# Kernel optimization log

Hardware: AMD Instinct MI355X
Metric: run time of the kernel (lower is better)

Reference implementation:

```python
import jax, jax.numpy as jnp
import numpy as np

B, T, N, D, H = 8, 24, 512, 128, 8
HD = D // H
HID = int(D * 2.0)
SCALES = (1.0, 0.01)


def _l2norm(a):
    # F.normalize(dim=-1), eps=1e-12
    n = jnp.sqrt(jnp.sum(a * a, axis=-1, keepdims=True))
    return a / jnp.maximum(n, 1e-12)


def _layernorm(a, g, b):
    mu = a.mean(-1, keepdims=True)
    var = ((a - mu) ** 2).mean(-1, keepdims=True)
    return (a - mu) / jnp.sqrt(var + 1e-5) * g + b


def _fast_attention_layer(z, qkv_w, out_w, out_b):
    # z: [B,T,N,D]; qkv_w: [D,3D]; out_w: [2D,D]; out_b: [D]
    b, t, n, d = z.shape
    q, k, v = jnp.split(z @ qkv_w, 3, axis=-1)          # each [B,T,N,D]
    q = q.reshape(b, t, n, H, HD)
    k = k.reshape(b, t, n, H, HD)
    v = v.reshape(b, t, n, H, HD)
    qn = _l2norm(q)
    kn = _l2norm(k)
    # spatial linear attention (tokens = nodes, axis 2)
    kvs = jnp.einsum('btnhm,btnhd->bthmd', kn, v)
    num = jnp.einsum('btnhm,bthmd->btnhd', qn, kvs) + n * v
    den = jnp.einsum('btnhm,bthm->btnh', qn, kn.sum(axis=2))[..., None] + n
    out_s = (num / den).reshape(b, t, n, d)
    # temporal linear attention (tokens = time steps, axis 1)
    kvt = jnp.einsum('btnhm,btnhd->bnhmd', kn, v)
    numt = jnp.einsum('btnhm,bnhmd->btnhd', qn, kvt) + t * v
    dent = jnp.einsum('btnhm,bnhm->btnh', qn, kn.sum(axis=1))[..., None] + t
    out_t = (numt / dent).reshape(b, t, n, d)
    return jnp.concatenate([out_s, out_t], axis=-1) @ out_w + out_b


def setup_inputs() -> dict:
    key = jax.random.key(0)
    ks = jax.random.split(key, 20)
    s = 0.02
    inp = {
        'x': jax.random.normal(ks[0], (B, T, N, D), jnp.float32),
        'graph': jax.random.uniform(ks[1], (T, N, N), jnp.float32) / N,
        'qkv_w0': jax.random.normal(ks[2], (D, 3 * D), jnp.float32) * s,
        'out_w0': jax.random.normal(ks[3], (2 * D, D), jnp.float32) * s,
        'out_b0': jnp.zeros((D,), jnp.float32),
        'pw_w0': jax.random.normal(ks[4], (D, D), jnp.float32) * s,
        'pw_b0': jax.random.normal(ks[5], (D,), jnp.float32) * s,
        'qkv_w1': jax.random.normal(ks[6], (D, 3 * D), jnp.float32) * s,
        'out_w1': jax.random.normal(ks[7], (2 * D, D), jnp.float32) * s,
        'out_b1': jnp.zeros((D,), jnp.float32),
        'pw_w1': jax.random.normal(ks[8], (D, D), jnp.float32) * s,
        'pw_b1': jax.random.normal(ks[9], (D,), jnp.float32) * s,
        'fc1_w': jax.random.normal(ks[10], (D, HID), jnp.float32) * s,
        'fc1_b': jnp.zeros((HID,), jnp.float32),
        'fc2_w': jax.random.normal(ks[11], (HID, D), jnp.float32) * s,
        'fc2_b': jnp.zeros((D,), jnp.float32),
        'ln1_g': jnp.ones((D,), jnp.float32),
        'ln1_b': jnp.zeros((D,), jnp.float32),
        'ln2_g': jnp.ones((D,), jnp.float32),
        'ln2_b': jnp.zeros((D,), jnp.float32),
    }
    return inp


def reference(x, graph, qkv_w0, out_w0, out_b0, pw_w0, pw_b0,
              qkv_w1, out_w1, out_b1, pw_w1, pw_b1,
              fc1_w, fc1_b, fc2_w, fc2_b, ln1_g, ln1_b, ln2_g, ln2_b):
    # GraphPropagate (Ks=order=2): x_loc = [x, graph @ x]; dropout in eval mode
    x1 = jnp.einsum('tni,btid->btnd', graph, x)
    x_loc = (x, x1)
    layer_params = ((qkv_w0, out_w0, out_b0, pw_w0, pw_b0),
                    (qkv_w1, out_w1, out_b1, pw_w1, pw_b1))
    c = x
    x_glo = x
    for k in range(2):
        qkv_w, out_w, out_b, pw_w, pw_b = layer_params[k]
        att = _fast_attention_layer(x_loc[k], qkv_w, out_w, out_b)
        pw = c @ pw_w + pw_b
        x_glo = x_glo + att * pw * SCALES[k]
        c = att
    h = _layernorm(x + x_glo, ln1_g, ln1_b)
    mlp = jax.nn.relu(h @ fc1_w + fc1_b) @ fc2_w + fc2_b
    return _layernorm(h + mlp, ln2_g, ln2_b)
```

## Files before the change

### kernel.cpp

```cpp
#include <hip/hip_runtime.h>
#include <cstddef>

#define Bb 8
#define Tt 24
#define Nn 512
#define Dd 128
#define Hh 8

typedef unsigned short u16;
using short8 = __attribute__((ext_vector_type(8))) short;
using f32x4  = __attribute__((ext_vector_type(4))) float;

__device__ __forceinline__ float b2f(u16 u) {
  union { unsigned u; float f; } w; w.u = ((unsigned)u) << 16; return w.f;
}
__device__ __forceinline__ u16 f2b(float f) {
  union { float f; unsigned u; } w; w.f = f;
  unsigned r = w.u + 0x7FFFu + ((w.u >> 16) & 1u);
  return (u16)(r >> 16);
}

__device__ __forceinline__ void gld16(const u16* g, u16* s) {
  __builtin_amdgcn_global_load_lds(
      (const __attribute__((address_space(1))) unsigned int*)g,
      (__attribute__((address_space(3))) unsigned int*)s, 16, 0, 0);
}

__device__ __forceinline__ void mm_phase(const u16* __restrict__ A,
                                         const u16* __restrict__ BT,
                                         int K, int m0,
                                         u16* sA, u16* sB, f32x4 acc[4][4])
{
  const int tid = threadIdx.x;
  const int l = tid & 63, wid = tid >> 6;
  const int wm = (wid >> 1) << 6, wn = (wid & 1) << 6;
  int a_off[4], b_off[4];
#pragma unroll
  for (int i = 0; i < 4; ++i) {
    a_off[i] = (wm + i * 16 + (l & 15)) * 64 + (l >> 4) * 16;
    b_off[i] = (wn + i * 16 + (l & 15)) * 64 + (l >> 4) * 16;
  }
  const int gr = l >> 2, kqo = (l & 3) * 8;
  const int R0 = wid * 32 + gr, R1 = wid * 32 + 16 + gr;
  u16* dA0 = sA + (wid * 2 + 0) * 512;
  u16* dA1 = sA + (wid * 2 + 1) * 512;
  u16* dB0 = sB + (wid * 2 + 0) * 512;
  u16* dB1 = sB + (wid * 2 + 1) * 512;
  const size_t aR0 = (size_t)(m0 + R0) * K, aR1 = (size_t)(m0 + R1) * K;
  const size_t bR0 = (size_t)R0 * K, bR1 = (size_t)R1 * K;
  for (int k0 = 0; k0 < K; k0 += 32) {
    __syncthreads();
    gld16(A + aR0 + k0 + kqo, dA0);
    gld16(A + aR1 + k0 + kqo, dA1);
    gld16(BT + bR0 + k0 + kqo, dB0);
    gld16(BT + bR1 + k0 + kqo, dB1);
    __syncthreads();
    short8 af[4], bf_[4];
#pragma unroll
    for (int i = 0; i < 4; ++i) {
      af[i]  = *(const short8*)((const char*)sA + a_off[i]);
      bf_[i] = *(const short8*)((const char*)sB + b_off[i]);
    }
#pragma unroll
    for (int mi = 0; mi < 4; ++mi)
#pragma unroll
      for (int ni = 0; ni < 4; ++ni)
        acc[mi][ni] = __builtin_amdgcn_mfma_f32_16x16x32_bf16(
            af[mi], bf_[ni], acc[mi][ni], 0, 0, 0);
  }
}

template <int OUTBF16, int RELU>
__device__ __forceinline__ void gemm_mfma_body(
    const u16* __restrict__ A, const u16* __restrict__ BT,
    const float* __restrict__ bias, void* __restrict__ Cv,
    int N, int K, int m0, int n0)
{
  __shared__ u16 sA[4096];
  __shared__ u16 sB[4096];
  f32x4 acc[4][4] = {};
  mm_phase(A, BT + (size_t)n0 * K, K, m0, sA, sB, acc);
  const int l = threadIdx.x & 63, wid = threadIdx.x >> 6;
  const int wm = (wid >> 1) << 6, wn = (wid & 1) << 6;
  const int cr = (l >> 4) << 2, cc = l & 15;
#pragma unroll
  for (int mi = 0; mi < 4; ++mi) {
    int rowb = m0 + wm + mi * 16 + cr;
#pragma unroll
    for (int ni = 0; ni < 4; ++ni) {
      int col = n0 + wn + ni * 16 + cc;
      float bb = bias ? bias[col] : 0.f;
#pragma unroll
      for (int r = 0; r < 4; ++r) {
        float v = acc[mi][ni][r] + bb;
        if (RELU) v = fmaxf(v, 0.f);
        size_t idx = (size_t)(rowb + r) * N + col;
        if (OUTBF16) ((u16*)Cv)[idx] = f2b(v);
        else         ((float*)Cv)[idx] = v;
      }
    }
  }
}

template <int OUTBF16, int RELU>
__global__ __launch_bounds__(256) void gemm_mfma_k(
    const u16* __restrict__ A, const u16* __restrict__ BT,
    const float* __restrict__ bias, void* __restrict__ C, int N, int K)
{
  gemm_mfma_body<OUTBF16, RELU>(A, BT, bias, C, N, K,
                                blockIdx.y * 128, blockIdx.x * 128);
}

__global__ __launch_bounds__(256) void gemm_mfma_graph(
    const u16* __restrict__ g, const u16* __restrict__ xT, u16* __restrict__ x1)
{
  const int bt = blockIdx.z, t = bt % Tt;
  gemm_mfma_body<1, 0>(g + (size_t)t * Nn * Nn, xT + (size_t)bt * Dd * Nn,
                       nullptr, x1 + (size_t)bt * Nn * Dd,
                       Dd, Nn, blockIdx.y * 128, 0);
}

__global__ __launch_bounds__(256) void gemm_og0(
    const u16* __restrict__ cat, const u16* __restrict__ outT, const float* __restrict__ ob,
    const u16* __restrict__ xb,  const u16* __restrict__ pwT,  const float* __restrict__ pb,
    u16* __restrict__ gp0, u16* __restrict__ att0)
{
  __shared__ u16 sA[4096], sB[4096];
  const int m0 = blockIdx.x * 128;
  f32x4 accP[4][4] = {};
  mm_phase(xb, pwT, 128, m0, sA, sB, accP);
  f32x4 accO[4][4] = {};
  mm_phase(cat, outT, 256, m0, sA, sB, accO);
  const int l = threadIdx.x & 63, wid = threadIdx.x >> 6;
  const int wm = (wid >> 1) << 6, wn = (wid & 1) << 6;
  const int cr = (l >> 4) << 2, cc = l & 15;
#pragma unroll
  for (int mi = 0; mi < 4; ++mi) {
    int rowb = m0 + wm + mi * 16 + cr;
#pragma unroll
    for (int ni = 0; ni < 4; ++ni) {
      int col = wn + ni * 16 + cc;
      float obv = ob[col], pbv = pb[col];
#pragma unroll
      for (int r = 0; r < 4; ++r) {
        size_t idx = (size_t)(rowb + r) * 128 + col;
        float attv = accO[mi][ni][r] + obv;
        float pwv  = accP[mi][ni][r] + pbv;
        att0[idx] = f2b(attv);
        gp0[idx] = f2b(attv * pwv);
      }
    }
  }
}

__global__ __launch_bounds__(256) void gemm_og1(
    const u16* __restrict__ cat, const u16* __restrict__ outT, const float* __restrict__ ob,
    const u16* __restrict__ att0, const u16* __restrict__ pwT, const float* __restrict__ pb,
    const u16* __restrict__ gp0, const float* __restrict__ x,
    const float* __restrict__ g, const float* __restrict__ be,
    u16* __restrict__ h16)
{
  __shared__ __align__(16) u16 smem[128 * 136];
  __shared__ float sg[128], sbt[128];
  u16* sA = smem;
  u16* sB = smem + 4096;
  if (threadIdx.x < 128) { sg[threadIdx.x] = g[threadIdx.x]; sbt[threadIdx.x] = be[threadIdx.x]; }
  const int m0 = blockIdx.x * 128;
  f32x4 accP[4][4] = {};
  mm_phase(att0, pwT, 128, m0, sA, sB, accP);
  f32x4 accO[4][4] = {};
  mm_phase(cat, outT, 256, m0, sA, sB, accO);
  const int l = threadIdx.x & 63, wid = threadIdx.x >> 6;
  const int wm = (wid >> 1) << 6, wn = (wid & 1) << 6;
  const int cr = (l >> 4) << 2, cc = l & 15;
  __syncthreads();
#pragma unroll
  for (int mi = 0; mi < 4; ++mi) {
    int lrow = wm + mi * 16 + cr;
#pragma unroll
    for (int ni = 0; ni < 4; ++ni) {
      int col = wn + ni * 16 + cc;
      float obv = ob[col], pbv = pb[col];
#pragma unroll
      for (int r = 0; r < 4; ++r) {
        size_t idx = (size_t)(m0 + lrow + r) * 128 + col;
        float attv = accO[mi][ni][r] + obv;
        float pwv  = accP[mi][ni][r] + pbv;
        float hpre = 2.f * x[idx] + b2f(gp0[idx]) + attv * pwv * 0.01f;
        smem[(lrow + r) * 136 + col] = f2b(hpre);
      }
    }
  }
  __syncthreads();
  const int row = threadIdx.x >> 1, half = threadIdx.x & 1;
  const u16* rp = smem + row * 136 + half * 64;
  float s = 0.f, ss = 0.f;
#pragma unroll
  for (int j8 = 0; j8 < 8; ++j8) {
    short8 v = *(const short8*)(rp + j8 * 8);
#pragma unroll
    for (int j = 0; j < 8; ++j) { float f = b2f((u16)v[j]); s += f; ss += f * f; }
  }
  s += __shfl_xor(s, 1);
  ss += __shfl_xor(ss, 1);
  float mu = s * (1.f / 128.f);
  float rstd = rsqrtf(ss * (1.f / 128.f) - mu * mu + 1e-5f);
  size_t gbase = (size_t)(m0 + row) * 128 + half * 64;
#pragma unroll
  for (int j8 = 0; j8 < 8; ++j8) {
    short8 v = *(const short8*)(rp + j8 * 8);
    short8 o;
#pragma unroll
    for (int j = 0; j < 8; ++j) {
      int col = half * 64 + j8 * 8 + j;
      o[j] = (short)f2b((b2f((u16)v[j]) - mu) * rstd * sg[col] + sbt[col]);
    }
    *(short8*)(h16 + gbase + j8 * 8) = o;
  }
}

__global__ __launch_bounds__(256) void gemm_fc2ln(
    const u16* __restrict__ hid, const u16* __restrict__ fc2T, const float* __restrict__ fb,
    const u16* __restrict__ h16, const float* __restrict__ g, const float* __restrict__ be,
    float* __restrict__ out)
{
  __shared__ __align__(16) u16 smem[128 * 136];
  __shared__ float sg[128], sbt[128];
  u16* sA = smem;
  u16* sB = smem + 4096;
  if (threadIdx.x < 128) { sg[threadIdx.x] = g[threadIdx.x]; sbt[threadIdx.x] = be[threadIdx.x]; }
  const int m0 = blockIdx.x * 128;
  f32x4 accO[4][4] = {};
  mm_phase(hid, fc2T, 256, m0, sA, sB, accO);
  const int l = threadIdx.x & 63, wid = threadIdx.x >> 6;
  const int wm = (wid >> 1) << 6, wn = (wid & 1) << 6;
  const int cr = (l >> 4) << 2, cc = l & 15;
  __syncthreads();
#pragma unroll
  for (int mi = 0; mi < 4; ++mi) {
    int lrow = wm + mi * 16 + cr;
#pragma unroll
    for (int ni = 0; ni < 4; ++ni) {
      int col = wn + ni * 16 + cc;
      float fbv = fb[col];
#pragma unroll
      for (int r = 0; r < 4; ++r) {
        size_t idx = (size_t)(m0 + lrow + r) * 128 + col;
        float hpre = b2f(h16[idx]) + accO[mi][ni][r] + fbv;
        smem[(lrow + r) * 136 + col] = f2b(hpre);
      }
    }
  }
  __syncthreads();
  const int row = threadIdx.x >> 1, half = threadIdx.x & 1;
  const u16* rp = smem + row * 136 + half * 64;
  float s = 0.f, ss = 0.f;
#pragma unroll
  for (int j8 = 0; j8 < 8; ++j8) {
    short8 v = *(const short8*)(rp + j8 * 8);
#pragma unroll
    for (int j = 0; j < 8; ++j) { float f = b2f((u16)v[j]); s += f; ss += f * f; }
  }
  s += __shfl_xor(s, 1);
  ss += __shfl_xor(ss, 1);
  float mu = s * (1.f / 128.f);
  float rstd = rsqrtf(ss * (1.f / 128.f) - mu * mu + 1e-5f);
  size_t gbase = (size_t)(m0 + row) * 128 + half * 64;
#pragma unroll
  for (int j8 = 0; j8 < 8; ++j8) {
    short8 v = *(const short8*)(rp + j8 * 8);
    float4 o0, o1;
#pragma unroll
    for (int j = 0; j < 8; ++j) {
      int col = half * 64 + j8 * 8 + j;
      float y = (b2f((u16)v[j]) - mu) * rstd * sg[col] + sbt[col];
      if (j < 4) ((float*)&o0)[j] = y; else ((float*)&o1)[j - 4] = y;
    }
    *(float4*)(out + gbase + j8 * 8) = o0;
    *(float4*)(out + gbase + j8 * 8 + 4) = o1;
  }
}

__global__ __launch_bounds__(256) void qknorm(const u16* __restrict__ qkv,
                                              float* __restrict__ inv, size_t nidx)
{
  size_t idx = (size_t)blockIdx.x * 256 + threadIdx.x;
  if (idx >= nidx) return;
  size_t row = idx >> 4;
  int g = (int)(idx & 15);
  const u16* p = qkv + row * 384 + g * 16;
  short8 a = *(const short8*)p;
  short8 b = *(const short8*)(p + 8);
  float ss = 0.f;
#pragma unroll
  for (int j = 0; j < 8; ++j) {
    float f0 = b2f((u16)a[j]), f1 = b2f((u16)b[j]);
    ss += f0 * f0 + f1 * f1;
  }
  inv[idx] = 1.f / fmaxf(sqrtf(ss), 1e-12f);
}

__global__ __launch_bounds__(256) void cvt_f32_bf16(const float* __restrict__ src,
                                                    u16* __restrict__ dst, size_t n8)
{
  size_t i = (size_t)blockIdx.x * 256 + threadIdx.x;
  if (i >= n8) return;
  const float4* s = (const float4*)src;
  float4 u = s[i * 2], v = s[i * 2 + 1];
  short8 o;
  o[0] = (short)f2b(u.x); o[1] = (short)f2b(u.y);
  o[2] = (short)f2b(u.z); o[3] = (short)f2b(u.w);
  o[4] = (short)f2b(v.x); o[5] = (short)f2b(v.y);
  o[6] = (short)f2b(v.z); o[7] = (short)f2b(v.w);
  *(short8*)(dst + i * 8) = o;
}

__global__ __launch_bounds__(256) void transpose_cvt(const float* __restrict__ src,
                                                     u16* __restrict__ dst,
                                                     int R, int C)
{
  __shared__ u16 tile[64][65];
  const int tid = threadIdx.x;
  src += (size_t)blockIdx.z * R * C;
  dst += (size_t)blockIdx.z * R * C;
  const int c0 = blockIdx.x * 64, r0 = blockIdx.y * 64;
  const int tx = tid & 63, ty = tid >> 6;
#pragma unroll
  for (int i = 0; i < 64; i += 4)
    tile[ty + i][tx] = f2b(src[(size_t)(r0 + ty + i) * C + c0 + tx]);
  __syncthreads();
#pragma unroll
  for (int i = 0; i < 64; i += 4)
    dst[(size_t)(c0 + ty + i) * R + r0 + tx] = tile[tx][ty + i];
}

__global__ __launch_bounds__(256) void cvt_transpose_x(const float* __restrict__ src,
                                                       u16* __restrict__ xb,
                                                       u16* __restrict__ xT)
{
  __shared__ u16 tile[64][65];
  const int tid = threadIdx.x;
  const size_t zo = (size_t)blockIdx.z * Nn * Dd;
  src += zo; xb += zo; xT += zo;
  const int c0 = blockIdx.x * 64, r0 = blockIdx.y * 64;
  const int tx = tid & 63, ty = tid >> 6;
#pragma unroll
  for (int i = 0; i < 64; i += 4) {
    u16 b = f2b(src[(size_t)(r0 + ty + i) * Dd + c0 + tx]);
    tile[ty + i][tx] = b;
    xb[(size_t)(r0 + ty + i) * Dd + c0 + tx] = b;
  }
  __syncthreads();
#pragma unroll
  for (int i = 0; i < 64; i += 4)
    xT[(size_t)(c0 + ty + i) * Nn + r0 + tx] = tile[tx][ty + i];
}

__global__ __launch_bounds__(256) void spatial_stats(const u16* __restrict__ qkv,
                                                     const float* __restrict__ qkn,
                                                     float* __restrict__ kvs2,
                                                     float* __restrict__ ksum)
{
  __shared__ u16 sKT[16 * 512];
  __shared__ u16 sVT[16 * 512];
  __shared__ float red[4][16][16];
  __shared__ float red2[4][16];
  const int bt = blockIdx.x, h = blockIdx.y;
  const int tid = threadIdx.x;

  u16 kr[2][16], vr[2][16];
#pragma unroll
  for (int r = 0; r < 2; ++r) {
    int n = tid * 2 + r;
    size_t rowg = (size_t)bt * 512 + n;
    size_t base = rowg * 384;
    float inv = qkn[rowg * 16 + 8 + h];
    short8 k0 = *(const short8*)(qkv + base + 128 + h * 16);
    short8 k1 = *(const short8*)(qkv + base + 136 + h * 16);
    short8 v0 = *(const short8*)(qkv + base + 256 + h * 16);
    short8 v1 = *(const short8*)(qkv + base + 264 + h * 16);
#pragma unroll
    for (int j = 0; j < 8; ++j) {
      kr[r][j]     = f2b(b2f((u16)k0[j]) * inv);
      kr[r][j + 8] = f2b(b2f((u16)k1[j]) * inv);
      vr[r][j] = (u16)v0[j]; vr[r][j + 8] = (u16)v1[j];
    }
  }
#pragma unroll
  for (int m = 0; m < 16; ++m) {
    unsigned pk = (unsigned)kr[0][m] | ((unsigned)kr[1][m] << 16);
    unsigned pv = (unsigned)vr[0][m] | ((unsigned)vr[1][m] << 16);
    int wa = ((m << 10) + (tid << 2)) ^ ((m & 7) << 4);
    *(unsigned*)((char*)sKT + wa) = pk;
    *(unsigned*)((char*)sVT + wa) = pv;
  }
  __syncthreads();

  const int l = tid & 63, w = tid >> 6;
  const int fr = l & 15, tq = l >> 4;
  short8 ones;
#pragma unroll
  for (int j = 0; j < 8; ++j) ones[j] = (short)0x3F80;
  f32x4 acc = {}, acs = {};
#pragma unroll
  for (int kk = 0; kk < 4; ++kk) {
    int noff = w * 128 + kk * 32 + tq * 8;
    int ra = ((fr << 10) + (noff << 1)) ^ ((fr & 7) << 4);
    short8 afr = *(const short8*)((const char*)sKT + ra);
    short8 bfr = *(const short8*)((const char*)sVT + ra);
    acc = __builtin_amdgcn_mfma_f32_16x16x32_bf16(afr, bfr, acc, 0, 0, 0);
    acs = __builtin_amdgcn_mfma_f32_16x16x32_bf16(afr, ones, acs, 0, 0, 0);
  }
#pragma unroll
  for (int r = 0; r < 4; ++r) red[w][tq * 4 + r][fr] = acc[r];
  if (fr == 0) {
#pragma unroll
    for (int r = 0; r < 4; ++r) red2[w][tq * 4 + r] = acs[r];
  }
  __syncthreads();
  const size_t o = (size_t)bt * 8 + h;
  {
    int m = tid >> 4, d = tid & 15;
    float s = red[0][m][d] + red[1][m][d] + red[2][m][d] + red[3][m][d];
    kvs2[o * 256 + d * 16 + m] = s;
  }
  if (tid < 16) {
    float s = red2[0][tid] + red2[1][tid] + red2[2][tid] + red2[3][tid];
    ksum[o * 16 + tid] = s;
  }
}

__global__ __launch_bounds__(256) void temporal_stats(const u16* __restrict__ qkv,
                                                      const float* __restrict__ qkn,
                                                      float* __restrict__ kvt,
                                                      float* __restrict__ kst)
{
  __shared__ u16 sKT[128 * 32];
  __shared__ u16 sVT[128 * 32];
  const int nn = blockIdx.x, b = blockIdx.y;
  const int tid = threadIdx.x;
  if (tid < 128) {
    short8 z = {};
    int wa = ((tid << 6) + 48) ^ ((tid & 3) << 4);
    *(short8*)((char*)sKT + wa) = z;
    *(short8*)((char*)sVT + wa) = z;
  }
  for (int idx = tid; idx < 384; idx += 256) {
    int t = idx >> 4, c8 = idx & 15;
    size_t rowg = ((size_t)(b * 24 + t) * 512) + nn;
    float inv = qkn[rowg * 16 + 8 + (c8 >> 1)];
    short8 kv = *(const short8*)(qkv + rowg * 384 + 128 + c8 * 8);
    short8 vv = *(const short8*)(qkv + rowg * 384 + 256 + c8 * 8);
#pragma unroll
    for (int j = 0; j < 8; ++j) {
      int c = c8 * 8 + j;
      int wa = ((c << 6) + (t << 1)) ^ ((c & 3) << 4);
      *(u16*)((char*)sKT + wa) = f2b(b2f((u16)kv[j]) * inv);
      *(u16*)((char*)sVT + wa) = (u16)vv[j];
    }
  }
  __syncthreads();
  const int l = tid & 63, w = tid >> 6;
  const int fr = l & 15, tq = l >> 4;
  const size_t nb = (size_t)b * 512 + nn;
  short8 ones;
#pragma unroll
  for (int j = 0; j < 8; ++j) ones[j] = (short)0x3F80;
#pragma unroll
  for (int hi = 0; hi < 2; ++hi) {
    int h = w * 2 + hi;
    int c = h * 16 + fr;
    int ra = ((c << 6) + (tq << 4)) ^ ((c & 3) << 4);
    short8 afr = *(const short8*)((const char*)sKT + ra);
    short8 bfr = *(const short8*)((const char*)sVT + ra);
    f32x4 z = {};
    f32x4 acc = __builtin_amdgcn_mfma_f32_16x16x32_bf16(afr, bfr, z, 0, 0, 0);
    f32x4 acs = __builtin_amdgcn_mfma_f32_16x16x32_bf16(afr, ones, z, 0, 0, 0);
#pragma unroll
    for (int r = 0; r < 4; ++r)
      kvt[nb * 2048 + (size_t)(tq * 4 + r) * 128 + h * 16 + fr] = acc[r];
    if (fr == 0) {
#pragma unroll
      for (int r = 0; r < 4; ++r)
        kst[(nb * 8 + h) * 16 + tq * 4 + r] = acs[r];
    }
  }
}

__global__ __launch_bounds__(256) void attn_apply(const u16* __restrict__ qkv,
                                                  const float* __restrict__ qkn,
                                                  const float* __restrict__ kvs2,
                                                  const float* __restrict__ kss,
                                                  const float* __restrict__ kvt,
                                                  const float* __restrict__ kst,
                                                  u16* __restrict__ out_cat)
{
  __shared__ float s_kvt[2][2048];
  const int nn0 = blockIdx.x * 2, b = blockIdx.y;
  const int t0 = blockIdx.z * 8;
  const int tid = threadIdx.x;
  const int sub = tid >> 7, cl = tid & 127;
  const int nn = nn0 + sub;
  const size_t nb = (size_t)b * 512 + nn;
  for (int i = cl; i < 2048; i += 128) s_kvt[sub][i] = kvt[nb * 2048 + i];
  __syncthreads();
  const int hh = cl >> 4, d = cl & 15;
  float kstr[16];
  {
    const float4* k4 = (const float4*)(kst + (nb * 8 + hh) * 16);
#pragma unroll
    for (int i = 0; i < 4; ++i) {
      float4 v = k4[i];
      kstr[i * 4] = v.x; kstr[i * 4 + 1] = v.y; kstr[i * 4 + 2] = v.z; kstr[i * 4 + 3] = v.w;
    }
  }
  for (int t = t0; t < t0 + 8; ++t) {
    const size_t row = ((size_t)(b * 24 + t) * 512) + nn;
    const u16* qp = qkv + row * 384 + hh * 16;
    short8 q0 = *(const short8*)qp;
    short8 q1 = *(const short8*)(qp + 8);
    const float inv = qkn[row * 16 + hh];
    float qf[16];
#pragma unroll
    for (int j = 0; j < 8; ++j) {
      qf[j] = b2f((u16)q0[j]);
      qf[j + 8] = b2f((u16)q1[j]);
    }
    const size_t hb = (size_t)(b * 24 + t) * 8 + hh;
    const float4* M4 = (const float4*)(kvs2 + hb * 256 + d * 16);
    float accs = 0.f;
#pragma unroll
    for (int i = 0; i < 4; ++i) {
      float4 m = M4[i];
      accs = fmaf(qf[i * 4], m.x, fmaf(qf[i * 4 + 1], m.y,
             fmaf(qf[i * 4 + 2], m.z, fmaf(qf[i * 4 + 3], m.w, accs))));
    }
    const float4* K4 = (const float4*)(kss + hb * 16);
    float dps = 0.f;
#pragma unroll
    for (int i = 0; i < 4; ++i) {
      float4 m = K4[i];
      dps = fmaf(qf[i * 4], m.x, fmaf(qf[i * 4 + 1], m.y,
            fmaf(qf[i * 4 + 2], m.z, fmaf(qf[i * 4 + 3], m.w, dps))));
    }
    float acct = 0.f, dpt = 0.f;
#pragma unroll
    for (int mI = 0; mI < 16; ++mI) {
      acct = fmaf(qf[mI], s_kvt[sub][mI * 128 + cl], acct);
      dpt  = fmaf(qf[mI], kstr[mI], dpt);
    }
    float vv = b2f(qkv[row * 384 + 256 + cl]);
    float rs = __builtin_amdgcn_rcpf(fmaf(dps, inv, 512.f));
    float rt = __builtin_amdgcn_rcpf(fmaf(dpt, inv, 24.f));
    out_cat[row * 256 + cl]       = f2b(fmaf(accs, inv, 512.f * vv) * rs);
    out_cat[row * 256 + 128 + cl] = f2b(fmaf(acct, inv, 24.f * vv) * rt);
  }
}

extern "C" void kernel_launch(void* const* d_in, const int* in_sizes, int n_in,
                              void* d_out, int out_size, void* d_ws, size_t ws_size,
                              hipStream_t stream)
{
  const float* x      = (const float*)d_in[0];
  const float* graph  = (const float*)d_in[1];
  const float* qkv_w0 = (const float*)d_in[2];
  const float* out_w0 = (const float*)d_in[3];
  const float* out_b0 = (const float*)d_in[4];
  const float* pw_w0  = (const float*)d_in[5];
  const float* pw_b0  = (const float*)d_in[6];
  const float* qkv_w1 = (const float*)d_in[7];
  const float* out_w1 = (const float*)d_in[8];
  const float* out_b1 = (const float*)d_in[9];
  const float* pw_w1  = (const float*)d_in[10];
  const float* pw_b1  = (const float*)d_in[11];
  const float* fc1_w  = (const float*)d_in[12];
  const float* fc1_b  = (const float*)d_in[13];
  const float* fc2_w  = (const float*)d_in[14];
  const float* fc2_b  = (const float*)d_in[15];
  const float* ln1_g  = (const float*)d_in[16];
  const float* ln1_b  = (const float*)d_in[17];
  const float* ln2_g  = (const float*)d_in[18];
  const float* ln2_b  = (const float*)d_in[19];
  float* out = (float*)d_out;

  auto al = [](size_t v) { return (v + 255) & ~(size_t)255; };
  const size_t Rb = 12288;
  const size_t fixed = al((size_t)Tt * Nn * Nn * 2) + 2 * al((size_t)384 * 128 * 2)
                     + 2 * al((size_t)128 * 256 * 2) + 2 * al((size_t)128 * 128 * 2)
                     + al((size_t)256 * 128 * 2) + al((size_t)128 * 256 * 2);
  const size_t perb = al(Rb * 768) + al(Rb * 512) + 4 * al(Rb * 256) + al(Rb * 512)
                    + al(Rb * 64)
                    + al((size_t)Tt * 8 * 256 * 4) + al((size_t)Tt * 8 * 16 * 4)
                    + al((size_t)Nn * 8 * 256 * 4) + al((size_t)Nn * 8 * 16 * 4);
  int CB = 8;
  while (CB > 1 && fixed + (size_t)CB * perb > ws_size) CB >>= 1;
  const size_t Mc = (size_t)CB * Rb;

  char* cur = (char*)d_ws;
  auto alloc = [&](size_t bytes) { char* p = cur; cur += (bytes + 255) & ~(size_t)255; return p; };
  u16* g_b16 = (u16*)alloc((size_t)Tt * Nn * Nn * 2);
  u16* qkvT0 = (u16*)alloc((size_t)384 * 128 * 2);
  u16* qkvT1 = (u16*)alloc((size_t)384 * 128 * 2);
  u16* outT0 = (u16*)alloc((size_t)128 * 256 * 2);
  u16* outT1 = (u16*)alloc((size_t)128 * 256 * 2);
  u16* pwT0  = (u16*)alloc((size_t)128 * 128 * 2);
  u16* pwT1  = (u16*)alloc((size_t)128 * 128 * 2);
  u16* fc1T  = (u16*)alloc((size_t)256 * 128 * 2);
  u16* fc2T  = (u16*)alloc((size_t)128 * 256 * 2);
  u16* qkvb  = (u16*)alloc(Mc * 768);
  u16* catb  = (u16*)alloc(Mc * 512);
  u16* x1b   = (u16*)alloc(Mc * 256);
  u16* att0  = (u16*)alloc(Mc * 256);
  u16* xb    = (u16*)alloc(Mc * 256);
  u16* xT    = (u16*)alloc(Mc * 256);
  u16* gp0   = (u16*)alloc(Mc * 512);
  float* qkn = (float*)alloc(Mc * 64);
  float* kvs = (float*)alloc((size_t)CB * Tt * 8 * 256 * 4);
  float* kss = (float*)alloc((size_t)CB * Tt * 8 * 16 * 4);
  float* kvt = (float*)alloc((size_t)CB * Nn * 8 * 256 * 4);
  float* kst = (float*)alloc((size_t)CB * Nn * 8 * 16 * 4);

  dim3 blk(256);
  cvt_f32_bf16<<<dim3((Tt * Nn * Nn / 8 + 255) / 256), blk, 0, stream>>>(
      graph, g_b16, (size_t)Tt * Nn * Nn / 8);
  transpose_cvt<<<dim3(6, 2, 1), blk, 0, stream>>>(qkv_w0, qkvT0, 128, 384);
  transpose_cvt<<<dim3(6, 2, 1), blk, 0, stream>>>(qkv_w1, qkvT1, 128, 384);
  transpose_cvt<<<dim3(2, 4, 1), blk, 0, stream>>>(out_w0, outT0, 256, 128);
  transpose_cvt<<<dim3(2, 4, 1), blk, 0, stream>>>(out_w1, outT1, 256, 128);
  transpose_cvt<<<dim3(2, 2, 1), blk, 0, stream>>>(pw_w0, pwT0, 128, 128);
  transpose_cvt<<<dim3(2, 2, 1), blk, 0, stream>>>(pw_w1, pwT1, 128, 128);
  transpose_cvt<<<dim3(4, 2, 1), blk, 0, stream>>>(fc1_w, fc1T, 128, 256);
  transpose_cvt<<<dim3(2, 4, 1), blk, 0, stream>>>(fc2_w, fc2T, 256, 128);

  const int MB = (int)(Mc / 128);
  const int nchunk = Bb / CB;
  for (int c = 0; c < nchunk; ++c) {
    const size_t off = (size_t)c * Mc * 128;
    const float* xc = x + off;
    float* outc = out + off;

    cvt_transpose_x<<<dim3(2, 8, CB * Tt), blk, 0, stream>>>(xc, xb, xT);
    gemm_mfma_graph<<<dim3(1, 4, CB * Tt), blk, 0, stream>>>(g_b16, xT, x1b);

    gemm_mfma_k<1, 0><<<dim3(3, MB), blk, 0, stream>>>(xb, qkvT0, nullptr, qkvb, 384, 128);
    qknorm<<<dim3((unsigned)(Mc / 16)), blk, 0, stream>>>(qkvb, qkn, Mc * 16);
    spatial_stats<<<dim3(CB * Tt, Hh), blk, 0, stream>>>(qkvb, qkn, kvs, kss);
    temporal_stats<<<dim3(Nn, CB), blk, 0, stream>>>(qkvb, qkn, kvt, kst);
    attn_apply<<<dim3(Nn / 2, CB, 3), blk, 0, stream>>>(qkvb, qkn, kvs, kss, kvt, kst, catb);
    gemm_og0<<<dim3(MB), blk, 0, stream>>>(catb, outT0, out_b0, xb, pwT0, pw_b0,
                                           gp0, att0);

    gemm_mfma_k<1, 0><<<dim3(3, MB), blk, 0, stream>>>(x1b, qkvT1, nullptr, qkvb, 384, 128);
    qknorm<<<dim3((unsigned)(Mc / 16)), blk, 0, stream>>>(qkvb, qkn, Mc * 16);
    spatial_stats<<<dim3(CB * Tt, Hh), blk, 0, stream>>>(qkvb, qkn, kvs, kss);
    temporal_stats<<<dim3(Nn, CB), blk, 0, stream>>>(qkvb, qkn, kvt, kst);
    attn_apply<<<dim3(Nn / 2, CB, 3), blk, 0, stream>>>(qkvb, qkn, kvs, kss, kvt, kst, catb);
    u16* h16 = qkvb;
    gemm_og1<<<dim3(MB), blk, 0, stream>>>(catb, outT1, out_b1, att0, pwT1, pw_b1,
                                           gp0, xc, ln1_g, ln1_b, h16);

    gemm_mfma_k<1, 1><<<dim3(2, MB), blk, 0, stream>>>(h16, fc1T, fc1_b, catb, 256, 128);
    gemm_fc2ln<<<dim3(MB), blk, 0, stream>>>(catb, fc2T, fc2_b, h16, ln2_g, ln2_b, outc);
  }

  (void)in_sizes; (void)n_in; (void)out_size;
}
```

Measured before the change: 678.8 us.

## Swizzle LDS GEMM staging via registers and split attn_apply by spatial/temporal half

The GEMM k-loop no longer uses direct global-to-LDS loads. Each thread loads into registers before the barrier and writes to LDS with an XOR swizzle, so fragment reads avoid bank conflicts and global latency overlaps the sync. attn_apply now handles one node per block, with one half of the threads computing the spatial output and the other half the temporal output. This halves per-thread work and shared memory but doubles the grid size and adds duplicate q loads and warp-level divergence.

```diff
diff --git a/kernel.cpp b/kernel.cpp
--- a/kernel.cpp
+++ b/kernel.cpp
@@ -20,12 +20,6 @@
   return (u16)(r >> 16);
 }
 
-__device__ __forceinline__ void gld16(const u16* g, u16* s) {
-  __builtin_amdgcn_global_load_lds(
-      (const __attribute__((address_space(1))) unsigned int*)g,
-      (__attribute__((address_space(3))) unsigned int*)s, 16, 0, 0);
-}
-
 __device__ __forceinline__ void mm_phase(const u16* __restrict__ A,
                                          const u16* __restrict__ BT,
                                          int K, int m0,
@@ -37,23 +31,28 @@
   int a_off[4], b_off[4];
 #pragma unroll
   for (int i = 0; i < 4; ++i) {
-    a_off[i] = (wm + i * 16 + (l & 15)) * 64 + (l >> 4) * 16;
-    b_off[i] = (wn + i * 16 + (l & 15)) * 64 + (l >> 4) * 16;
-  }
-  const int gr = l >> 2, kqo = (l & 3) * 8;
-  const int R0 = wid * 32 + gr, R1 = wid * 32 + 16 + gr;
-  u16* dA0 = sA + (wid * 2 + 0) * 512;
-  u16* dA1 = sA + (wid * 2 + 1) * 512;
-  u16* dB0 = sB + (wid * 2 + 0) * 512;
-  u16* dB1 = sB + (wid * 2 + 1) * 512;
-  const size_t aR0 = (size_t)(m0 + R0) * K, aR1 = (size_t)(m0 + R1) * K;
-  const size_t bR0 = (size_t)R0 * K, bR1 = (size_t)R1 * K;
+    int ra = wm + i * 16 + (l & 15);
+    a_off[i] = ((ra << 6) + ((l >> 4) << 4)) ^ ((ra & 7) << 4);
+    int rb = wn + i * 16 + (l & 15);
+    b_off[i] = ((rb << 6) + ((l >> 4) << 4)) ^ ((rb & 7) << 4);
+  }
+  const int r0 = tid >> 2, s0 = tid & 3;
+  const int r1 = r0 + 64;
+  const int w0 = ((r0 << 6) + (s0 << 4)) ^ ((r0 & 7) << 4);
+  const int w1 = ((r1 << 6) + (s0 << 4)) ^ ((r1 & 7) << 4);
+  const size_t aR0 = (size_t)(m0 + r0) * K, aR1 = (size_t)(m0 + r1) * K;
+  const size_t bR0 = (size_t)r0 * K, bR1 = (size_t)r1 * K;
+  const int ks = s0 * 8;
   for (int k0 = 0; k0 < K; k0 += 32) {
+    short8 a0 = *(const short8*)(A + aR0 + k0 + ks);
+    short8 a1 = *(const short8*)(A + aR1 + k0 + ks);
+    short8 b0 = *(const short8*)(BT + bR0 + k0 + ks);
+    short8 b1 = *(const short8*)(BT + bR1 + k0 + ks);
     __syncthreads();
-    gld16(A + aR0 + k0 + kqo, dA0);
-    gld16(A + aR1 + k0 + kqo, dA1);
-    gld16(BT + bR0 + k0 + kqo, dB0);
-    gld16(BT + bR1 + k0 + kqo, dB1);
+    *(short8*)((char*)sA + w0) = a0;
+    *(short8*)((char*)sA + w1) = a1;
+    *(short8*)((char*)sB + w0) = b0;
+    *(short8*)((char*)sB + w1) = b1;
     __syncthreads();
     short8 af[4], bf_[4];
 #pragma unroll
@@ -495,18 +494,17 @@
                                                   const float* __restrict__ kst,
                                                   u16* __restrict__ out_cat)
 {
-  __shared__ float s_kvt[2][2048];
-  const int nn0 = blockIdx.x * 2, b = blockIdx.y;
+  __shared__ float s_kvt[2048];
+  const int nn = blockIdx.x, b = blockIdx.y;
   const int t0 = blockIdx.z * 8;
   const int tid = threadIdx.x;
+  const size_t nb = (size_t)b * 512 + nn;
+  for (int i = tid; i < 2048; i += 256) s_kvt[i] = kvt[nb * 2048 + i];
+  __syncthreads();
   const int sub = tid >> 7, cl = tid & 127;
-  const int nn = nn0 + sub;
-  const size_t nb = (size_t)b * 512 + nn;
-  for (int i = cl; i < 2048; i += 128) s_kvt[sub][i] = kvt[nb * 2048 + i];
-  __syncthreads();
   const int hh = cl >> 4, d = cl & 15;
   float kstr[16];
-  {
+  if (sub) {
     const float4* k4 = (const float4*)(kst + (nb * 8 + hh) * 16);
 #pragma unroll
     for (int i = 0; i < 4; ++i) {
@@ -526,34 +524,37 @@
       qf[j] = b2f((u16)q0[j]);
       qf[j + 8] = b2f((u16)q1[j]);
     }
-    const size_t hb = (size_t)(b * 24 + t) * 8 + hh;
-    const float4* M4 = (const float4*)(kvs2 + hb * 256 + d * 16);
-    float accs = 0.f;
-#pragma unroll
-    for (int i = 0; i < 4; ++i) {
-      float4 m = M4[i];
-      accs = fmaf(qf[i * 4], m.x, fmaf(qf[i * 4 + 1], m.y,
-             fmaf(qf[i * 4 + 2], m.z, fmaf(qf[i * 4 + 3], m.w, accs))));
-    }
-    const float4* K4 = (const float4*)(kss + hb * 16);
-    float dps = 0.f;
-#pragma unroll
-    for (int i = 0; i < 4; ++i) {
-      float4 m = K4[i];
-      dps = fmaf(qf[i * 4], m.x, fmaf(qf[i * 4 + 1], m.y,
-            fmaf(qf[i * 4 + 2], m.z, fmaf(qf[i * 4 + 3], m.w, dps))));
-    }
-    float acct = 0.f, dpt = 0.f;
-#pragma unroll
-    for (int mI = 0; mI < 16; ++mI) {
-      acct = fmaf(qf[mI], s_kvt[sub][mI * 128 + cl], acct);
-      dpt  = fmaf(qf[mI], kstr[mI], dpt);
-    }
     float vv = b2f(qkv[row * 384 + 256 + cl]);
-    float rs = __builtin_amdgcn_rcpf(fmaf(dps, inv, 512.f));
-    float rt = __builtin_amdgcn_rcpf(fmaf(dpt, inv, 24.f));
-    out_cat[row * 256 + cl]       = f2b(fmaf(accs, inv, 512.f * vv) * rs);
-    out_cat[row * 256 + 128 + cl] = f2b(fmaf(acct, inv, 24.f * vv) * rt);
+    if (!sub) {
+      const size_t hb = (size_t)(b * 24 + t) * 8 + hh;
+      const float4* M4 = (const float4*)(kvs2 + hb * 256 + d * 16);
+      float accs = 0.f;
+#pragma unroll
+      for (int i = 0; i < 4; ++i) {
+        float4 m = M4[i];
+        accs = fmaf(qf[i * 4], m.x, fmaf(qf[i * 4 + 1], m.y,
+               fmaf(qf[i * 4 + 2], m.z, fmaf(qf[i * 4 + 3], m.w, accs))));
+      }
+      const float4* K4 = (const float4*)(kss + hb * 16);
+      float dps = 0.f;
+#pragma unroll
+      for (int i = 0; i < 4; ++i) {
+        float4 m = K4[i];
+        dps = fmaf(qf[i * 4], m.x, fmaf(qf[i * 4 + 1], m.y,
+              fmaf(qf[i * 4 + 2], m.z, fmaf(qf[i * 4 + 3], m.w, dps))));
+      }
+      float rs = __builtin_amdgcn_rcpf(fmaf(dps, inv, 512.f));
+      out_cat[row * 256 + cl] = f2b(fmaf(accs, inv, 512.f * vv) * rs);
+    } else {
+      float acct = 0.f, dpt = 0.f;
+#pragma unroll
+      for (int mI = 0; mI < 16; ++mI) {
+        acct = fmaf(qf[mI], s_kvt[mI * 128 + cl], acct);
+        dpt  = fmaf(qf[mI], kstr[mI], dpt);
+      }
+      float rt = __builtin_amdgcn_rcpf(fmaf(dpt, inv, 24.f));
+      out_cat[row * 256 + 128 + cl] = f2b(fmaf(acct, inv, 24.f * vv) * rt);
+    }
   }
 }
 
@@ -646,7 +647,7 @@
     qknorm<<<dim3((unsigned)(Mc / 16)), blk, 0, stream>>>(qkvb, qkn, Mc * 16);
     spatial_stats<<<dim3(CB * Tt, Hh), blk, 0, stream>>>(qkvb, qkn, kvs, kss);
     temporal_stats<<<dim3(Nn, CB), blk, 0, stream>>>(qkvb, qkn, kvt, kst);
-    attn_apply<<<dim3(Nn / 2, CB, 3), blk, 0, stream>>>(qkvb, qkn, kvs, kss, kvt, kst, catb);
+    attn_apply<<<dim3(Nn, CB, 3), blk, 0, stream>>>(qkvb, qkn, kvs, kss, kvt, kst, catb);
     gemm_og0<<<dim3(MB), blk, 0, stream>>>(catb, outT0, out_b0, xb, pwT0, pw_b0,
                                            gp0, att0);
 
@@ -654,7 +655,7 @@
     qknorm<<<dim3((unsigned)(Mc / 16)), blk, 0, stream>>>(qkvb, qkn, Mc * 16);
     spatial_stats<<<dim3(CB * Tt, Hh), blk, 0, stream>>>(qkvb, qkn, kvs, kss);
     temporal_stats<<<dim3(Nn, CB), blk, 0, stream>>>(qkvb, qkn, kvt, kst);
-    attn_apply<<<dim3(Nn / 2, CB, 3), blk, 0, stream>>>(qkvb, qkn, kvs, kss, kvt, kst, catb);
+    attn_apply<<<dim3(Nn, CB, 3), blk, 0, stream>>>(qkvb, qkn, kvs, kss, kvt, kst, catb);
     u16* h16 = qkvb;
     gemm_og1<<<dim3(MB), blk, 0, stream>>>(catb, outT1, out_b1, att0, pwT1, pw_b1,
                                            gp0, xc, ln1_g, ln1_b, h16);
```

Measured after the change: 695.2 us. +2.4%, slower.
